# Performance work log

Measured on AMD Instinct MI355X. Metric: run time of the kernel, lower is better.

Reference implementation:

```python
import jax, jax.numpy as jnp
import numpy as np

RADIUS = 2
TEMP = 1.0
B, CIN, D, H, W = 1, 32, 64, 64, 64
PROJ, OUT = 64, 64
K = (2 * RADIUS + 1) ** 3  # 125 local offsets

_OFFSETS = np.array([(dz, dy, dx)
                     for dz in range(-RADIUS, RADIUS + 1)
                     for dy in range(-RADIUS, RADIUS + 1)
                     for dx in range(-RADIUS, RADIUS + 1)], dtype=np.int32)


def _conv3d(x, w, b, pad):
    y = jax.lax.conv_general_dilated(
        x, w, window_strides=(1, 1, 1), padding=[(pad, pad)] * 3,
        dimension_numbers=('NCDHW', 'OIDHW', 'NCDHW'))
    if b is not None:
        y = y + b[None, :, None, None, None]
    return y


def _l2norm(x):
    # torch F.normalize(dim=1): x / max(||x||_2, 1e-12)
    n = jnp.sqrt(jnp.sum(x * x, axis=1, keepdims=True))
    return x / jnp.maximum(n, 1e-12)


def _inorm(x, eps=1e-5):
    # InstanceNorm3d (affine=False): normalize over spatial dims per (B,C)
    mu = jnp.mean(x, axis=(2, 3, 4), keepdims=True)
    var = jnp.mean((x - mu) ** 2, axis=(2, 3, 4), keepdims=True)
    return (x - mu) * jax.lax.rsqrt(var + eps)


def _ntn(x):
    return jnp.nan_to_num(x, nan=0.0, posinf=0.0, neginf=0.0)


def setup_inputs() -> dict:
    key = jax.random.key(0)
    ks = jax.random.split(key, 8)
    s = 0.05
    return {
        'source_features': jax.random.normal(ks[0], (B, CIN, D, H, W), jnp.float32),
        'warped_target_features': jax.random.normal(ks[1], (B, CIN, D, H, W), jnp.float32),
        'w_src': jax.random.normal(ks[2], (PROJ, CIN, 1, 1, 1), jnp.float32) * s,
        'b_src': jnp.zeros((PROJ,), jnp.float32),
        'w_tgt': jax.random.normal(ks[3], (PROJ, CIN, 1, 1, 1), jnp.float32) * s,
        'b_tgt': jnp.zeros((PROJ,), jnp.float32),
        'w_enc1': jax.random.normal(ks[4], (OUT, K + 5, 3, 3, 3), jnp.float32) * s,
        'b_enc1': jnp.zeros((OUT,), jnp.float32),
        'w_enc2': jax.random.normal(ks[5], (OUT, OUT, 3, 3, 3), jnp.float32) * s,
        'b_enc2': jnp.zeros((OUT,), jnp.float32),
    }


def reference(source_features, warped_target_features, w_src, b_src, w_tgt, b_tgt,
              w_enc1, b_enc1, w_enc2, b_enc2):
    sp = _l2norm(_conv3d(source_features, w_src, b_src, 0))      # [B,P,D,H,W]
    tp = _l2norm(_conv3d(warped_target_features, w_tgt, b_tgt, 0))
    pt = jnp.pad(tp, ((0, 0), (0, 0), (RADIUS, RADIUS), (RADIUS, RADIUS), (RADIUS, RADIUS)),
                 mode='edge')  # replicate pad

    starts = jnp.asarray(_OFFSETS + RADIUS, jnp.int32)  # [K,3] slice starts

    def corr_one(st):
        sh = jax.lax.dynamic_slice(pt, (0, 0, st[0], st[1], st[2]), (B, PROJ, D, H, W))
        return jnp.sum(sp * sh, axis=1)  # [B,D,H,W]

    corr = jnp.transpose(jax.vmap(corr_one)(starts), (1, 0, 2, 3, 4))  # [B,K,D,H,W]
    scaled = corr / max(TEMP, 1e-6)

    top2 = jax.lax.top_k(jnp.moveaxis(scaled, 1, -1), 2)[0]  # [B,D,H,W,2]
    m = jnp.moveaxis(top2[..., 0:1], -1, 1)   # running max   [B,1,D,H,W]
    s2 = jnp.moveaxis(top2[..., 1:2], -1, 1)  # second max

    p = jnp.exp(scaled - m)                    # [B,K,D,H,W]
    Z = jnp.sum(p, axis=1, keepdims=True)
    inv = 1.0 / jnp.maximum(Z, 1e-8)

    offv = jnp.asarray(_OFFSETS, jnp.float32)  # [K,3]
    expected_offset = _ntn(jnp.einsum('bkdhw,kc->bcdhw', p, offv) * inv)
    confidence = _ntn(jnp.minimum(inv, 1.0))   # max-prob = exp(m-m)/Z
    second_prob = jnp.exp(s2 - m) * inv
    margin = _ntn(jnp.maximum(confidence - second_prob, 0.0))
    entropy = _ntn(m + jnp.log(jnp.maximum(Z, 1e-8))
                   - jnp.sum(p * scaled, axis=1, keepdims=True) * inv)

    enc_in = jnp.concatenate([corr, expected_offset, confidence, entropy], axis=1)  # [B,K+5,D,H,W]
    h = _conv3d(enc_in, w_enc1, b_enc1, 1)
    h = jax.nn.gelu(_inorm(h), approximate=False)
    h = _conv3d(h, w_enc2, b_enc2, 1)
    h = jax.nn.gelu(_inorm(h), approximate=False)
    encoded_features = _ntn(h)

    return expected_offset, confidence, margin, entropy, encoded_features
```

## Files before the change

kernel.cpp:

```cpp
#include <hip/hip_runtime.h>

#define DEV __device__ __forceinline__

typedef short bf16x8 __attribute__((ext_vector_type(8)));
typedef float f32x4 __attribute__((ext_vector_type(4)));

static const int NVOX = 262144;

DEV float bflo(unsigned int u) { return __uint_as_float(u << 16); }
DEV float bfhi(unsigned int u) { return __uint_as_float(u & 0xffff0000u); }
DEV float bf2f(unsigned short s) { return __uint_as_float(((unsigned int)s) << 16); }
DEV unsigned short f2bf(float f) {
    unsigned int x = __float_as_uint(f);
    x += 0x7fffu + ((x >> 16) & 1u);
    return (unsigned short)(x >> 16);
}
DEV float ldin(const void* p, int i, int f) {
    return f ? ((const float*)p)[i] : bf2f(((const unsigned short*)p)[i]);
}

__global__ void sniff_kernel(const unsigned short* __restrict__ src, int* __restrict__ flag) {
    __shared__ int cnt[256];
    int t = threadIdx.x;
    int c = 0;
    for (int i = t; i < 4096; i += 256) {
        unsigned int u = (unsigned int)src[i] & 0x7fffu;
        c += (u >= 0x4900u) ? 1 : 0;
    }
    cnt[t] = c;
    __syncthreads();
    for (int s = 128; s > 0; s >>= 1) {
        if (t < s) cnt[t] += cnt[t + s];
        __syncthreads();
    }
    if (t == 0) *flag = (cnt[0] > 8) ? 1 : 0;
}

__global__ void prep_kernel(const void* __restrict__ w1, const void* __restrict__ w2,
                            const void* __restrict__ bsv, const void* __restrict__ btv,
                            const void* __restrict__ b1v, const void* __restrict__ b2v,
                            const int* __restrict__ flag,
                            unsigned short* __restrict__ Wf1,
                            unsigned short* __restrict__ Wf2,
                            float* __restrict__ fbias) {
    const int f = *flag;
    int idx = blockIdx.x * 256 + threadIdx.x;
    const int N1 = 27 * 5 * 4 * 512;
    const int N2 = 27 * 2 * 4 * 512;
    if (idx < N1) {
        int frag = idx >> 9;
        int r    = idx & 511;
        int lane = r >> 3, j = r & 7;
        int nt = frag & 3;
        int tk = frag >> 2;
        int tap = tk / 5, kc = tk % 5;
        int o  = nt * 16 + (lane & 15);
        int cp = kc * 32 + (lane >> 4) * 8 + j;
        unsigned short val = 0;
        if (cp < 130) val = f2bf(ldin(w1, (o * 130 + cp) * 27 + tap, f));
        Wf1[idx] = val;
    } else if (idx < N1 + N2) {
        int i2 = idx - N1;
        int frag = i2 >> 9;
        int r    = i2 & 511;
        int lane = r >> 3, j = r & 7;
        int nt = frag & 3;
        int tk = frag >> 2;
        int tap = tk >> 1, kc = tk & 1;
        int o = nt * 16 + (lane & 15);
        int c = kc * 32 + (lane >> 4) * 8 + j;
        Wf2[i2] = f2bf(ldin(w2, (o * 64 + c) * 27 + tap, f));
    } else if (idx < N1 + N2 + 256) {
        int j = idx - N1 - N2;
        const void* bp = (j < 64) ? bsv : (j < 128) ? btv : (j < 192) ? b1v : b2v;
        fbias[j] = ldin(bp, j & 63, f);
    }
}

__global__ __launch_bounds__(256) void proj_kernel(
        const void* __restrict__ Xsrc, const void* __restrict__ Xtgt,
        const void* __restrict__ Wsrc, const void* __restrict__ Wtgt,
        const float* __restrict__ fbias, const int* __restrict__ flag,
        unsigned short* __restrict__ SP, unsigned short* __restrict__ TP) {
    const int f = *flag;
    const void* Xin = blockIdx.y ? Xtgt : Xsrc;
    const void* W   = blockIdx.y ? Wtgt : Wsrc;
    const float* Bb = fbias + (blockIdx.y ? 64 : 0);
    unsigned short* Outp = blockIdx.y ? TP : SP;

    __shared__ float ws[2048];
    const int t = threadIdx.x;
    for (int i = t; i < 2048; i += 256) {
        int ci = i >> 6, o = i & 63;
        ws[i] = ldin(W, o * 32 + ci, f);
    }
    __syncthreads();

    const size_t v = (size_t)blockIdx.x * 256 + t;
    float acc[64];
#pragma unroll
    for (int o = 0; o < 64; ++o) acc[o] = Bb[o];
    if (f) {
        const float* Xf = (const float*)Xin;
        for (int ci = 0; ci < 32; ++ci) {
            float x = Xf[(size_t)ci * NVOX + v];
            const float4* wr = (const float4*)(ws + ci * 64);
#pragma unroll
            for (int o4 = 0; o4 < 16; ++o4) {
                float4 w4 = wr[o4];
                acc[o4 * 4 + 0] = fmaf(w4.x, x, acc[o4 * 4 + 0]);
                acc[o4 * 4 + 1] = fmaf(w4.y, x, acc[o4 * 4 + 1]);
                acc[o4 * 4 + 2] = fmaf(w4.z, x, acc[o4 * 4 + 2]);
                acc[o4 * 4 + 3] = fmaf(w4.w, x, acc[o4 * 4 + 3]);
            }
        }
    } else {
        const unsigned short* Xb = (const unsigned short*)Xin;
        for (int ci = 0; ci < 32; ++ci) {
            float x = bf2f(Xb[(size_t)ci * NVOX + v]);
            const float4* wr = (const float4*)(ws + ci * 64);
#pragma unroll
            for (int o4 = 0; o4 < 16; ++o4) {
                float4 w4 = wr[o4];
                acc[o4 * 4 + 0] = fmaf(w4.x, x, acc[o4 * 4 + 0]);
                acc[o4 * 4 + 1] = fmaf(w4.y, x, acc[o4 * 4 + 1]);
                acc[o4 * 4 + 2] = fmaf(w4.z, x, acc[o4 * 4 + 2]);
                acc[o4 * 4 + 3] = fmaf(w4.w, x, acc[o4 * 4 + 3]);
            }
        }
    }
    float s = 0.f;
#pragma unroll
    for (int o = 0; o < 64; ++o) s = fmaf(acc[o], acc[o], s);
    float scale = 1.f / fmaxf(sqrtf(s), 1e-12f);

    unsigned int pk[32];
#pragma unroll
    for (int o = 0; o < 32; ++o)
        pk[o] = (unsigned int)f2bf(acc[2 * o] * scale) |
                ((unsigned int)f2bf(acc[2 * o + 1] * scale) << 16);
    uint4* outp = (uint4*)(Outp + v * 64);
#pragma unroll
    for (int j = 0; j < 8; ++j)
        outp[j] = make_uint4(pk[4 * j], pk[4 * j + 1], pk[4 * j + 2], pk[4 * j + 3]);
}

DEV void tp_load(const unsigned short* __restrict__ TP, int t, int z, int y,
                 int it, uint4* pre) {
    const int zc = min(max(z + it / 5 - 2, 0), 63);
    const int yc = min(max(y + it % 5 - 2, 0), 63);
    const unsigned short* tbase = TP + ((size_t)zc * 64 + yc) * 4096;
#pragma unroll
    for (int j = 0; j < 3; ++j) {
        int i = t + j * 256;
        uint4 vv = make_uint4(0u, 0u, 0u, 0u);
        if (i < 640) {
            int pp = i >> 3, cc = i & 7;
            int xc = min(max(pp - 2, 0), 63);
            vv = *(const uint4*)(tbase + xc * 64 + cc * 8);
        }
        pre[j] = vv;
    }
}

DEV void tp_commit(unsigned short* buf, int t, const uint4* pre) {
#pragma unroll
    for (int j = 0; j < 3; ++j) {
        int i = t + j * 256;
        if (i < 640) {
            int pp = i >> 3, cc = i & 7;
            *(uint4*)((char*)buf + pp * 128 + ((cc ^ (pp & 7)) * 16)) = pre[j];
        }
    }
}

__global__ __launch_bounds__(256) void corr_kernel(
        const unsigned short* __restrict__ SP, const unsigned short* __restrict__ TP,
        unsigned short* __restrict__ X1, float* __restrict__ Out) {
    __shared__ __align__(16) unsigned short spb[64 * 64];
    __shared__ __align__(16) unsigned short tpb[2][80 * 64];
    __shared__ __align__(16) unsigned short stage[64 * 168];
    __shared__ __align__(16) float band[64 * 5];

    const int t = threadIdx.x;
    const int wv = t >> 6, lane = t & 63;
    const int q = lane >> 4, l16 = lane & 15;
    const int x0 = wv * 16;

    const int bid = blockIdx.x;
    const int wg = (bid & 7) * 512 + (bid >> 3);
    const int z = wg >> 6, y = wg & 63;
    const size_t vbase = ((size_t)z * 64 + y) * 64;

    uint4 spv0, spv1;
    {
        int i0 = t, i1 = t + 256;
        spv0 = *(const uint4*)(SP + (vbase + (i0 >> 3)) * 64 + (i0 & 7) * 8);
        spv1 = *(const uint4*)(SP + (vbase + (i1 >> 3)) * 64 + (i1 & 7) * 8);
    }
    {
        int vox = t >> 2, c4 = t & 3;
        *(uint4*)(&stage[vox * 168 + 128 + c4 * 8]) = make_uint4(0u, 0u, 0u, 0u);
    }
    {
        int i0 = t, i1 = t + 256;
        int xa = i0 >> 3, ca = i0 & 7;
        int xb = i1 >> 3, cb = i1 & 7;
        *(uint4*)((char*)spb + xa * 128 + ((ca ^ (xa & 7)) * 16)) = spv0;
        *(uint4*)((char*)spb + xb * 128 + ((cb ^ (xb & 7)) * 16)) = spv1;
    }

    float m = -1e30f, s2 = -1e30f, Zs = 0.f, S1 = 0.f, Ox = 0.f, Oy = 0.f, Oz = 0.f;

    uint4 pre[3];
    tp_load(TP, t, z, y, 0, pre);
    int p = 0;
    for (int it = 0; it < 25; ++it) {
        tp_commit(tpb[p], t, pre);
        __syncthreads();
        if (it < 24) tp_load(TP, t, z, y, it + 1, pre);

        f32x4 acc[2] = {{0.f, 0.f, 0.f, 0.f}, {0.f, 0.f, 0.f, 0.f}};
        {
            const char* sb = (const char*)spb;
            const char* tb = (const char*)tpb[p];
            const int xr = x0 + l16;
#pragma unroll
            for (int kc = 0; kc < 2; ++kc) {
                bf16x8 a = *(const bf16x8*)(sb + xr * 128 + (((kc * 4 + q) ^ (xr & 7)) * 16));
#pragma unroll
                for (int nt = 0; nt < 2; ++nt) {
                    const int pr = x0 + nt * 16 + l16;
                    bf16x8 b = *(const bf16x8*)(tb + pr * 128 + (((kc * 4 + q) ^ (pr & 7)) * 16));
                    acc[nt] = __builtin_amdgcn_mfma_f32_16x16x32_bf16(a, b, acc[nt], 0, 0, 0);
                }
            }
        }
        const int kb = it * 5;
#pragma unroll
        for (int nt = 0; nt < 2; ++nt) {
#pragma unroll
            for (int r = 0; r < 4; ++r) {
                int ml = q * 4 + r;
                int dxp = nt * 16 + l16 - ml;
                if ((unsigned)dxp < 5u) {
                    int xl = x0 + ml;
                    float d = acc[nt][r];
                    band[xl * 5 + dxp] = d;
                    stage[xl * 168 + kb + dxp] = f2bf(d);
                }
            }
        }
        __syncthreads();
        if (t < 64) {
            const float fz = (float)(it / 5 - 2), fy = (float)(it % 5 - 2);
#pragma unroll
            for (int dxp = 0; dxp < 5; ++dxp) {
                float d = band[t * 5 + dxp];
                float fx = (float)(dxp - 2);
                if (d > m) {
                    float sc = __expf(m - d);
                    Zs = fmaf(Zs, sc, 1.f); S1 = fmaf(S1, sc, d);
                    Ox = fmaf(Ox, sc, fx); Oy = fmaf(Oy, sc, fy); Oz = fmaf(Oz, sc, fz);
                    s2 = m; m = d;
                } else {
                    float e = __expf(d - m);
                    Zs += e; S1 = fmaf(e, d, S1);
                    Ox = fmaf(e, fx, Ox); Oy = fmaf(e, fy, Oy); Oz = fmaf(e, fz, Oz);
                    s2 = fmaxf(s2, d);
                }
            }
        }
        p ^= 1;
    }

    if (t < 64) {
        float inv  = 1.f / fmaxf(Zs, 1e-8f);
        float eoz = Oz * inv, eoy = Oy * inv, eox = Ox * inv;
        float conf = fminf(inv, 1.f);
        float marg = fmaxf(conf - __expf(s2 - m) * inv, 0.f);
        float ent  = m + __logf(fmaxf(Zs, 1e-8f)) - S1 * inv;
        stage[t * 168 + 125] = f2bf(eoz);
        stage[t * 168 + 126] = f2bf(eoy);
        stage[t * 168 + 127] = f2bf(eox);
        stage[t * 168 + 128] = f2bf(conf);
        stage[t * 168 + 129] = f2bf(ent);
        const size_t v = vbase + t;
        Out[v]                    = eoz;
        Out[(size_t)NVOX + v]     = eoy;
        Out[(size_t)2 * NVOX + v] = eox;
        Out[(size_t)3 * NVOX + v] = conf;
        Out[(size_t)4 * NVOX + v] = marg;
        Out[(size_t)5 * NVOX + v] = ent;
    }
    __syncthreads();

#pragma unroll
    for (int j = 0; j < 5; ++j) {
        int i = t + j * 256;
        int vox = i / 20, cc = i % 20;
        *(uint4*)(X1 + (vbase + vox) * 160 + (size_t)cc * 8) =
            *(const uint4*)(&stage[vox * 168 + cc * 8]);
    }
}

template <int CPAD, int LSTRIDE, int KC, int NLD>
__global__ __launch_bounds__(256) void conv3_kernel(
        const unsigned short* __restrict__ Xin, const unsigned short* __restrict__ Wf,
        const float* __restrict__ Bias, unsigned short* __restrict__ Out) {
    __shared__ unsigned short rowbuf[2][66 * LSTRIDE];
    const int lin = blockIdx.x;
    const int z = (lin & 7) * 8 + ((lin >> 3) >> 6);
    const int y = (lin >> 3) & 63;
    const int t = threadIdx.x;
    const int wv = t >> 6, lane = t & 63;
    const int quad = lane >> 4, l16 = lane & 15;
    const int mt2 = (wv & 1) * 2;
    const int nt2 = (wv >> 1) * 2;
    const int CH16 = CPAD / 8;

    f32x4 acc[2][2] = {{{0.f,0.f,0.f,0.f},{0.f,0.f,0.f,0.f}},
                       {{0.f,0.f,0.f,0.f},{0.f,0.f,0.f,0.f}}};

    uint4 pre[NLD];
    {
        const int zz = z - 1, yy = y - 1;
        const bool valid = (unsigned)zz < 64u && (unsigned)yy < 64u;
        const unsigned short* base = Xin + (((size_t)(valid ? zz : 0) * 64 + (valid ? yy : 0)) * 64) * CPAD;
#pragma unroll
        for (int i = 0; i < NLD; ++i) {
            int idx = t + i * 256;
            uint4 val = make_uint4(0u, 0u, 0u, 0u);
            if (idx < 66 * CH16) {
                int xi = idx / CH16, ci = idx % CH16;
                int gx = xi - 1;
                if (valid && gx >= 0 && gx < 64) val = *(const uint4*)(base + gx * CPAD + ci * 8);
            }
            pre[i] = val;
        }
    }

    int p = 0;
    for (int it = 0; it < 9; ++it) {
#pragma unroll
        for (int i = 0; i < NLD; ++i) {
            int idx = t + i * 256;
            if (idx < 66 * CH16) {
                int xi = idx / CH16, ci = idx % CH16;
                *(uint4*)(&rowbuf[p][xi * LSTRIDE + ci * 8]) = pre[i];
            }
        }
        __syncthreads();
        if (it < 8) {
            const int itn = it + 1;
            const int zz = z + itn / 3 - 1, yy = y + itn % 3 - 1;
            const bool valid = (unsigned)zz < 64u && (unsigned)yy < 64u;
            const unsigned short* base = Xin + (((size_t)(valid ? zz : 0) * 64 + (valid ? yy : 0)) * 64) * CPAD;
#pragma unroll
            for (int i = 0; i < NLD; ++i) {
                int idx = t + i * 256;
                uint4 val = make_uint4(0u, 0u, 0u, 0u);
                if (idx < 66 * CH16) {
                    int xi = idx / CH16, ci = idx % CH16;
                    int gx = xi - 1;
                    if (valid && gx >= 0 && gx < 64) val = *(const uint4*)(base + gx * CPAD + ci * 8);
                }
                pre[i] = val;
            }
        }
        const unsigned short* rp = rowbuf[p];
#pragma unroll
        for (int dx = 0; dx < 3; ++dx) {
            const int tap = it * 3 + dx;
            const unsigned short* wt = Wf + ((size_t)tap * KC * 4) * 512 + lane * 8;
            bf16x8 bf[KC][2];
#pragma unroll
            for (int kc = 0; kc < KC; ++kc)
#pragma unroll
                for (int nl = 0; nl < 2; ++nl)
                    bf[kc][nl] = *(const bf16x8*)(wt + (size_t)(kc * 4 + nt2 + nl) * 512);
#pragma unroll
            for (int kc = 0; kc < KC; ++kc) {
#pragma unroll
                for (int ml = 0; ml < 2; ++ml) {
                    bf16x8 a = *(const bf16x8*)(&rp[((mt2 + ml) * 16 + l16 + dx) * LSTRIDE + kc * 32 + quad * 8]);
#pragma unroll
                    for (int nl = 0; nl < 2; ++nl)
                        acc[ml][nl] = __builtin_amdgcn_mfma_f32_16x16x32_bf16(a, bf[kc][nl], acc[ml][nl], 0, 0, 0);
                }
            }
        }
        p ^= 1;
    }

    const size_t vbase = ((size_t)z * 64 + y) * 64;
#pragma unroll
    for (int ml = 0; ml < 2; ++ml) {
#pragma unroll
        for (int nl = 0; nl < 2; ++nl) {
            const int oc = (nt2 + nl) * 16 + l16;
            const float bv = Bias[oc];
#pragma unroll
            for (int r = 0; r < 4; ++r)
                Out[(vbase + (mt2 + ml) * 16 + quad * 4 + r) * 64 + oc] = f2bf(acc[ml][nl][r] + bv);
        }
    }
}

__global__ __launch_bounds__(256) void stats_kernel(
        const unsigned short* __restrict__ H, float* __restrict__ stats) {
    const int t = threadIdx.x;
    const int c = t & 63, g = t >> 6;
    float s = 0.f, q = 0.f;
    for (int v = blockIdx.x * 4 + g; v < NVOX; v += gridDim.x * 4) {
        float x = bf2f(H[(size_t)v * 64 + c]);
        s += x; q = fmaf(x, x, q);
    }
    __shared__ float ls[256], lq[256];
    ls[t] = s; lq[t] = q;
    __syncthreads();
    if (t < 64) {
        s = ls[t] + ls[t + 64] + ls[t + 128] + ls[t + 192];
        q = lq[t] + lq[t + 64] + lq[t + 128] + lq[t + 192];
        atomicAdd(&stats[c], s);
        atomicAdd(&stats[64 + c], q);
    }
}

__global__ void finalize_kernel(const float* __restrict__ stats, float* __restrict__ musr) {
    int c = threadIdx.x;
    if (c < 64) {
        float mu  = stats[c] * (1.0f / 262144.0f);
        float var = stats[64 + c] * (1.0f / 262144.0f) - mu * mu;
        musr[c] = mu;
        musr[64 + c] = rsqrtf(var + 1e-5f);
    }
}

__global__ __launch_bounds__(256) void norm_gelu_kernel(
        const unsigned short* __restrict__ H, const float* __restrict__ musr,
        unsigned short* __restrict__ G) {
    const size_t base = ((size_t)blockIdx.x * 256 + threadIdx.x) * 8;
    uint4 u = *(const uint4*)(H + base);
    const int c0 = (int)(base & 63);
    const unsigned int uu[4] = {u.x, u.y, u.z, u.w};
    unsigned int w[4];
#pragma unroll
    for (int p = 0; p < 4; ++p) {
        int c = c0 + p * 2;
        float x0 = (bflo(uu[p]) - musr[c]) * musr[64 + c];
        float x1 = (bfhi(uu[p]) - musr[c + 1]) * musr[64 + c + 1];
        float g0 = 0.5f * x0 * (1.f + erff(x0 * 0.70710678118f));
        float g1 = 0.5f * x1 * (1.f + erff(x1 * 0.70710678118f));
        w[p] = (unsigned int)f2bf(g0) | ((unsigned int)f2bf(g1) << 16);
    }
    *(uint4*)(G + base) = make_uint4(w[0], w[1], w[2], w[3]);
}

__global__ __launch_bounds__(256) void out_final_kernel(
        const unsigned short* __restrict__ H2, const float* __restrict__ musr,
        float* __restrict__ OutEnc) {
    __shared__ float tile[64 * 260];
    const int t = threadIdx.x;
    const size_t v0 = (size_t)blockIdx.x * 256;
#pragma unroll
    for (int i = 0; i < 8; ++i) {
        int chunk = t + i * 256;
        uint4 u = *(const uint4*)(H2 + v0 * 64 + (size_t)chunk * 8);
        int vox = chunk >> 3;
        int c0 = (chunk & 7) * 8;
        const unsigned int uu[4] = {u.x, u.y, u.z, u.w};
#pragma unroll
        for (int p = 0; p < 4; ++p) {
            int c = c0 + p * 2;
            float x0 = (bflo(uu[p]) - musr[c]) * musr[64 + c];
            float x1 = (bfhi(uu[p]) - musr[c + 1]) * musr[64 + c + 1];
            tile[c * 260 + vox]       = 0.5f * x0 * (1.f + erff(x0 * 0.70710678118f));
            tile[(c + 1) * 260 + vox] = 0.5f * x1 * (1.f + erff(x1 * 0.70710678118f));
        }
    }
    __syncthreads();
    const int c = t >> 2, sub = t & 3;
#pragma unroll
    for (int iter = 0; iter < 16; ++iter) {
        int fq = iter * 4 + sub;
        float4 val = *(const float4*)(&tile[c * 260 + fq * 4]);
        *(float4*)(OutEnc + (size_t)c * NVOX + v0 + fq * 4) = val;
    }
}

extern "C" void kernel_launch(void* const* d_in, const int* in_sizes, int n_in,
                              void* d_out, int out_size, void* d_ws, size_t ws_size,
                              hipStream_t stream) {
    const void* src  = d_in[0];
    const void* tgt  = d_in[1];
    const void* wsrc = d_in[2];
    const void* bsrc = d_in[3];
    const void* wtgt = d_in[4];
    const void* btgt = d_in[5];
    const void* w1   = d_in[6];
    const void* b1   = d_in[7];
    const void* w2   = d_in[8];
    const void* b2   = d_in[9];
    float* out = (float*)d_out;

    char* ws = (char*)d_ws;
    unsigned short* TPb = (unsigned short*)(ws);
    unsigned short* SPb = (unsigned short*)(ws + 33554432);
    unsigned short* X1  = (unsigned short*)(ws + 67108864);
    unsigned short* Wf1 = (unsigned short*)(ws + 150994944);
    unsigned short* Wf2 = (unsigned short*)(ws + 151547904);
    int*   flag   = (int*)  (ws + 151769088);
    float* fbias  = (float*)(ws + 151769152);
    float* stats1 = (float*)(ws + 151770176);
    float* musr1  = (float*)(ws + 151770688);
    float* stats2 = (float*)(ws + 151771200);
    float* musr2  = (float*)(ws + 151771712);
    unsigned short* H1 = SPb;
    unsigned short* G1 = TPb;
    unsigned short* H2 = X1;

    (void)hipMemsetAsync(stats1, 0, 2048, stream);
    sniff_kernel<<<1, 256, 0, stream>>>((const unsigned short*)src, flag);
    prep_kernel<<<1513, 256, 0, stream>>>(w1, w2, bsrc, btgt, b1, b2, flag, Wf1, Wf2, fbias);
    proj_kernel<<<dim3(1024, 2), 256, 0, stream>>>(src, tgt, wsrc, wtgt, fbias, flag, SPb, TPb);
    corr_kernel<<<4096, 256, 0, stream>>>(SPb, TPb, X1, out);
    conv3_kernel<160, 168, 5, 6><<<4096, 256, 0, stream>>>(X1, Wf1, fbias + 128, H1);
    stats_kernel<<<256, 256, 0, stream>>>(H1, stats1);
    finalize_kernel<<<1, 64, 0, stream>>>(stats1, musr1);
    norm_gelu_kernel<<<8192, 256, 0, stream>>>(H1, musr1, G1);
    conv3_kernel<64, 72, 2, 3><<<4096, 256, 0, stream>>>(G1, Wf2, fbias + 192, H2);
    stats_kernel<<<256, 256, 0, stream>>>(H2, stats2);
    finalize_kernel<<<1, 64, 0, stream>>>(stats2, musr2);
    out_final_kernel<<<1024, 256, 0, stream>>>(H2, musr2, out + 6 * (size_t)NVOX);
}
```

Before: 858.3 us.

## Split conv1 input channels into 128-channel main path plus packed tail GEMM

The first 3x3x3 conv previously padded its 130 input channels to 160 (5 K-chunks per tap), wasting MFMA work on zero padding. Now the main loop handles only 128 channels (4 K-chunks), and the 2 leftover channels across all 27 taps are packed into a single 64-wide K dimension processed by a separate small MFMA pass up front, using re-laid-out weights. This cuts padded MFMA work and shared-memory row size at the cost of an extra gather of scattered 2-channel values and an additional sync phase.

```diff
diff --git a/kernel.cpp b/kernel.cpp
--- a/kernel.cpp
+++ b/kernel.cpp
@@ -45,22 +45,35 @@
                             float* __restrict__ fbias) {
     const int f = *flag;
     int idx = blockIdx.x * 256 + threadIdx.x;
-    const int N1 = 27 * 5 * 4 * 512;
-    const int N2 = 27 * 2 * 4 * 512;
+    const int N1  = 27 * 4 * 4 * 512;
+    const int N1E = 2 * 4 * 512;
+    const int N2  = 27 * 2 * 4 * 512;
     if (idx < N1) {
         int frag = idx >> 9;
         int r    = idx & 511;
         int lane = r >> 3, j = r & 7;
         int nt = frag & 3;
         int tk = frag >> 2;
-        int tap = tk / 5, kc = tk % 5;
+        int tap = tk >> 2, kc = tk & 3;
         int o  = nt * 16 + (lane & 15);
         int cp = kc * 32 + (lane >> 4) * 8 + j;
+        Wf1[idx] = f2bf(ldin(w1, (o * 130 + cp) * 27 + tap, f));
+    } else if (idx < N1 + N1E) {
+        int i2 = idx - N1;
+        int frag = i2 >> 9;
+        int r    = i2 & 511;
+        int lane = r >> 3, j = r & 7;
+        int nt = frag & 3, kc = frag >> 2;
+        int o   = nt * 16 + (lane & 15);
+        int kap = kc * 32 + (lane >> 4) * 8 + j;
         unsigned short val = 0;
-        if (cp < 130) val = f2bf(ldin(w1, (o * 130 + cp) * 27 + tap, f));
+        if (kap < 54) {
+            int tap = kap >> 1, ch = 128 + (kap & 1);
+            val = f2bf(ldin(w1, (o * 130 + ch) * 27 + tap, f));
+        }
         Wf1[idx] = val;
-    } else if (idx < N1 + N2) {
-        int i2 = idx - N1;
+    } else if (idx < N1 + N1E + N2) {
+        int i2 = idx - N1 - N1E;
         int frag = i2 >> 9;
         int r    = i2 & 511;
         int lane = r >> 3, j = r & 7;
@@ -70,8 +83,8 @@
         int o = nt * 16 + (lane & 15);
         int c = kc * 32 + (lane >> 4) * 8 + j;
         Wf2[i2] = f2bf(ldin(w2, (o * 64 + c) * 27 + tap, f));
-    } else if (idx < N1 + N2 + 256) {
-        int j = idx - N1 - N2;
+    } else if (idx < N1 + N1E + N2 + 256) {
+        int j = idx - N1 - N1E - N2;
         const void* bp = (j < 64) ? bsv : (j < 128) ? btv : (j < 192) ? b1v : b2v;
         fbias[j] = ldin(bp, j & 63, f);
     }
@@ -304,9 +317,10 @@
     }
 }
 
-template <int CPAD, int LSTRIDE, int KC, int NLD>
+template <int XSTRIDE, int CPAD, int LSTRIDE, int KC, int NLD, bool TAIL>
 __global__ __launch_bounds__(256) void conv3_kernel(
         const unsigned short* __restrict__ Xin, const unsigned short* __restrict__ Wf,
+        const unsigned short* __restrict__ Wfe,
         const float* __restrict__ Bias, unsigned short* __restrict__ Out) {
     __shared__ unsigned short rowbuf[2][66 * LSTRIDE];
     const int lin = blockIdx.x;
@@ -326,7 +340,7 @@
     {
         const int zz = z - 1, yy = y - 1;
         const bool valid = (unsigned)zz < 64u && (unsigned)yy < 64u;
-        const unsigned short* base = Xin + (((size_t)(valid ? zz : 0) * 64 + (valid ? yy : 0)) * 64) * CPAD;
+        const unsigned short* base = Xin + (((size_t)(valid ? zz : 0) * 64 + (valid ? yy : 0)) * 64) * XSTRIDE;
 #pragma unroll
         for (int i = 0; i < NLD; ++i) {
             int idx = t + i * 256;
@@ -334,10 +348,47 @@
             if (idx < 66 * CH16) {
                 int xi = idx / CH16, ci = idx % CH16;
                 int gx = xi - 1;
-                if (valid && gx >= 0 && gx < 64) val = *(const uint4*)(base + gx * CPAD + ci * 8);
+                if (valid && gx >= 0 && gx < 64) val = *(const uint4*)(base + gx * XSTRIDE + ci * 8);
             }
             pre[i] = val;
         }
+    }
+
+    if (TAIL) {
+        unsigned short* ebuf = &rowbuf[1][0];
+#pragma unroll
+        for (int i2 = 0; i2 < 8; ++i2) {
+            int i = t + i2 * 256;
+            int vox = i >> 5, slot = i & 31;
+            unsigned int val = 0u;
+            int kap;
+            if (slot < 27) {
+                int dz = slot / 9 - 1, dy = (slot / 3) % 3 - 1, dxx = slot % 3 - 1;
+                int zz = z + dz, yy = y + dy, xx = vox + dxx;
+                kap = slot * 2;
+                if ((unsigned)zz < 64u && (unsigned)yy < 64u && (unsigned)xx < 64u)
+                    val = *(const unsigned int*)(Xin + (((size_t)zz * 64 + yy) * 64 + xx) * XSTRIDE + 128);
+            } else {
+                kap = 54 + (slot - 27) * 2;
+            }
+            *(unsigned int*)(ebuf + vox * 72 + kap) = val;
+        }
+        __syncthreads();
+#pragma unroll
+        for (int kc = 0; kc < 2; ++kc) {
+            bf16x8 bte[2];
+#pragma unroll
+            for (int nl = 0; nl < 2; ++nl)
+                bte[nl] = *(const bf16x8*)(Wfe + (size_t)(kc * 4 + nt2 + nl) * 512 + lane * 8);
+#pragma unroll
+            for (int ml = 0; ml < 2; ++ml) {
+                bf16x8 a = *(const bf16x8*)(ebuf + ((mt2 + ml) * 16 + l16) * 72 + (kc * 4 + quad) * 8);
+#pragma unroll
+                for (int nl = 0; nl < 2; ++nl)
+                    acc[ml][nl] = __builtin_amdgcn_mfma_f32_16x16x32_bf16(a, bte[nl], acc[ml][nl], 0, 0, 0);
+            }
+        }
+        __syncthreads();
     }
 
     int p = 0;
@@ -355,7 +406,7 @@
             const int itn = it + 1;
             const int zz = z + itn / 3 - 1, yy = y + itn % 3 - 1;
             const bool valid = (unsigned)zz < 64u && (unsigned)yy < 64u;
-            const unsigned short* base = Xin + (((size_t)(valid ? zz : 0) * 64 + (valid ? yy : 0)) * 64) * CPAD;
+            const unsigned short* base = Xin + (((size_t)(valid ? zz : 0) * 64 + (valid ? yy : 0)) * 64) * XSTRIDE;
 #pragma unroll
             for (int i = 0; i < NLD; ++i) {
                 int idx = t + i * 256;
@@ -363,7 +414,7 @@
                 if (idx < 66 * CH16) {
                     int xi = idx / CH16, ci = idx % CH16;
                     int gx = xi - 1;
-                    if (valid && gx >= 0 && gx < 64) val = *(const uint4*)(base + gx * CPAD + ci * 8);
+                    if (valid && gx >= 0 && gx < 64) val = *(const uint4*)(base + gx * XSTRIDE + ci * 8);
                 }
                 pre[i] = val;
             }
@@ -519,17 +570,18 @@
     unsigned short* H1 = SPb;
     unsigned short* G1 = TPb;
     unsigned short* H2 = X1;
+    unsigned short* Wf1e = Wf1 + 27 * 4 * 4 * 512;
 
     (void)hipMemsetAsync(stats1, 0, 2048, stream);
     sniff_kernel<<<1, 256, 0, stream>>>((const unsigned short*)src, flag);
-    prep_kernel<<<1513, 256, 0, stream>>>(w1, w2, bsrc, btgt, b1, b2, flag, Wf1, Wf2, fbias);
+    prep_kernel<<<1313, 256, 0, stream>>>(w1, w2, bsrc, btgt, b1, b2, flag, Wf1, Wf2, fbias);
     proj_kernel<<<dim3(1024, 2), 256, 0, stream>>>(src, tgt, wsrc, wtgt, fbias, flag, SPb, TPb);
     corr_kernel<<<4096, 256, 0, stream>>>(SPb, TPb, X1, out);
-    conv3_kernel<160, 168, 5, 6><<<4096, 256, 0, stream>>>(X1, Wf1, fbias + 128, H1);
+    conv3_kernel<160, 128, 136, 4, 5, true><<<4096, 256, 0, stream>>>(X1, Wf1, Wf1e, fbias + 128, H1);
     stats_kernel<<<256, 256, 0, stream>>>(H1, stats1);
     finalize_kernel<<<1, 64, 0, stream>>>(stats1, musr1);
     norm_gelu_kernel<<<8192, 256, 0, stream>>>(H1, musr1, G1);
-    conv3_kernel<64, 72, 2, 3><<<4096, 256, 0, stream>>>(G1, Wf2, fbias + 192, H2);
+    conv3_kernel<64, 64, 72, 2, 3, false><<<4096, 256, 0, stream>>>(G1, Wf2, nullptr, fbias + 192, H2);
     stats_kernel<<<256, 256, 0, stream>>>(H2, stats2);
     finalize_kernel<<<1, 64, 0, stream>>>(stats2, musr2);
     out_final_kernel<<<1024, 256, 0, stream>>>(H2, musr2, out + 6 * (size_t)NVOX);
```

Result: faster. 794.3 us (-7.5%).
